# Optimization experiments

Hardware: AMD Instinct MI355X
Metric: run time of the kernel (lower is better)

Reference implementation:

```python
import jax, jax.numpy as jnp
from jax import lax
import numpy as np

THRESHOLD = 0.8
SECONDARY = 0.6
SECONDARY_WEIGHT = 0.5
BN_EPS = 1e-5


def _conv_relu_pool(x, W, b):
    # x: [B,C,H,W], W: [O,I,3,3]
    y = lax.conv_general_dilated(x, W, window_strides=(1, 1), padding='SAME',
                                 dimension_numbers=('NCHW', 'OIHW', 'NCHW'))
    y = y + b[None, :, None, None]
    y = jax.nn.relu(y)
    return lax.reduce_window(y, -jnp.inf, lax.max, (1, 1, 2, 2), (1, 1, 2, 2), 'VALID')


def setup_inputs() -> dict:
    key = jax.random.key(0)
    ks = jax.random.split(key, 12)
    B, H, W = 1024, 64, 64
    d0, d1, d2 = 4096, 1024, 256  # qnn_arch
    inp = {}
    inp['x'] = jax.random.normal(ks[0], (B, 1, H, W), dtype=jnp.float32)
    # conv params (kaiming-ish scaling)
    inp['cw1'] = jax.random.normal(ks[1], (8, 1, 3, 3), jnp.float32) * (1.0 / np.sqrt(1 * 9))
    inp['cb1'] = jax.random.normal(ks[2], (8,), jnp.float32) * 0.01
    inp['cw2'] = jax.random.normal(ks[3], (16, 8, 3, 3), jnp.float32) * (1.0 / np.sqrt(8 * 9))
    inp['cb2'] = jax.random.normal(ks[4], (16,), jnp.float32) * 0.01
    # linear layers of the 'graph QNN'
    inp['w1'] = jax.random.normal(ks[5], (d1, d0), jnp.float32) * (1.0 / np.sqrt(d0))
    inp['b1'] = jax.random.normal(ks[6], (d1,), jnp.float32) * 0.01
    inp['w2'] = jax.random.normal(ks[7], (d2, d1), jnp.float32) * (1.0 / np.sqrt(d1))
    inp['b2'] = jax.random.normal(ks[8], (d2,), jnp.float32) * 0.01
    # BatchNorm1d affine params
    inp['gamma'] = jnp.ones((d2,), jnp.float32)
    inp['beta'] = jnp.zeros((d2,), jnp.float32)
    return inp


def reference(x, cw1, cb1, cw2, cb2, w1, b1, w2, b2, gamma, beta):
    B = x.shape[0]
    # CNN feature extractor
    feat = _conv_relu_pool(x, cw1, cb1)
    feat = _conv_relu_pool(feat, cw2, cb2)
    flat = feat.reshape(B, -1)                      # [B, 4096]
    # graph-QNN layers with tanh
    h1 = jnp.tanh(flat @ w1.T + b1)                 # [B, 1024]
    last = jnp.tanh(h1 @ w2.T + b2)                 # [B, 256]
    # fidelity adjacency: vectorized normalize + Gram + squared cosine
    norms = jnp.linalg.norm(last, axis=1, keepdims=True)  # [B,1]
    nrm = last / (norms + 1e-12)
    fid = (nrm @ nrm.T) ** 2                        # [B, B]
    adj = jnp.where(fid >= THRESHOLD, 1.0,
                    jnp.where(fid >= SECONDARY, SECONDARY_WEIGHT, 0.0))
    adj = adj * (1.0 - jnp.eye(B, dtype=adj.dtype))  # no self-edges
    # BatchNorm1d (training mode: batch statistics, biased variance)
    mean = jnp.mean(last, axis=0)
    var = jnp.mean((last - mean) ** 2, axis=0)
    out = (last - mean) / jnp.sqrt(var + BN_EPS) * gamma + beta
    return out, adj
```

## Files before the change

### kernel.cpp

```cpp
#include <hip/hip_runtime.h>
#include <hip/hip_bf16.h>
#include <math.h>


typedef double f64x4 __attribute__((ext_vector_type(4)));

__global__ __launch_bounds__(256) void conv1_kernel(
    const float* __restrict__ x, const float* __restrict__ cw1,
    const float* __restrict__ cb1, float* __restrict__ feat1) {
  __shared__ float sX[66 * 66];
  __shared__ float sW1[72];
  __shared__ float sB1[8];

  const int b = blockIdx.x;
  const int t = threadIdx.x;

  for (int i = t; i < 66 * 66; i += 256) sX[i] = 0.0f;
  if (t < 72) sW1[t] = cw1[t];
  if (t < 8)  sB1[t] = cb1[t];
  __syncthreads();

  const float* xb = x + (size_t)b * 4096;
  for (int i = t; i < 4096; i += 256)
    sX[((i >> 6) + 1) * 66 + (i & 63) + 1] = xb[i];
  __syncthreads();

  for (int task = t; task < 2048; task += 256) {
    const int ch = task >> 8;
    const int rem = task & 255;
    const int py = rem >> 3;
    const int px0 = (rem & 7) * 4;

    double w9[9];
#pragma unroll
    for (int k = 0; k < 9; ++k) w9[k] = (double)sW1[ch * 9 + k];

    float reg[4][10];
#pragma unroll
    for (int r = 0; r < 4; ++r)
#pragma unroll
      for (int c = 0; c < 5; ++c) {
        const float2 v =
            *(const float2*)&sX[(2 * py + r) * 66 + 2 * px0 + 2 * c];
        reg[r][2 * c] = v.x;
        reg[r][2 * c + 1] = v.y;
      }

    float out4[4];
#pragma unroll
    for (int px = 0; px < 4; ++px) {
      double best = -1e300;
#pragma unroll
      for (int dy = 0; dy < 2; ++dy) {
#pragma unroll
        for (int dx = 0; dx < 2; ++dx) {
          double s = 0.0;
#pragma unroll
          for (int ky = 0; ky < 3; ++ky)
#pragma unroll
            for (int kx = 0; kx < 3; ++kx)
              s = fma((double)reg[dy + ky][2 * px + dx + kx], w9[ky * 3 + kx],
                      s);
          best = fmax(best, s);
        }
      }
      out4[px] = (float)fmax(best + (double)sB1[ch], 0.0);
    }
    *(float4*)&feat1[(size_t)b * 8192 + ch * 1024 + py * 32 + px0] =
        make_float4(out4[0], out4[1], out4[2], out4[3]);
  }
}

__global__ __launch_bounds__(256) void conv2_kernel(
    const float* __restrict__ feat1, const float* __restrict__ cw2,
    const float* __restrict__ cb2, float* __restrict__ flat) {
  __shared__ float sF[8 * 34 * 34];
  __shared__ float sW2[1152];
  __shared__ float sB2[16];

  const int b = blockIdx.x;
  const int t = threadIdx.x;

  for (int i = t; i < 8 * 34 * 34; i += 256) sF[i] = 0.0f;
  for (int i = t; i < 1152; i += 256) sW2[i] = cw2[i];
  if (t < 16) sB2[t] = cb2[t];
  __syncthreads();

  const float* fb = feat1 + (size_t)b * 8192;
  for (int i = t; i < 8192; i += 256) {
    const int ch = i >> 10, pos = i & 1023;
    sF[ch * 1156 + ((pos >> 5) + 1) * 34 + (pos & 31) + 1] = fb[i];
  }
  __syncthreads();

  const int py = t >> 4, px = t & 15;
  float* ob = flat + (size_t)b * 4096 + py * 16 + px;

#pragma unroll 1
  for (int oh = 0; oh < 2; ++oh) {
    double acc[8][4];
#pragma unroll
    for (int o = 0; o < 8; ++o)
#pragma unroll
      for (int q = 0; q < 4; ++q) acc[o][q] = 0.0;

#pragma unroll
    for (int ic = 0; ic < 8; ++ic) {
      float r[4][4];
#pragma unroll
      for (int iy = 0; iy < 4; ++iy) {
        const float2 v0 =
            *(const float2*)&sF[ic * 1156 + (2 * py + iy) * 34 + 2 * px];
        const float2 v1 =
            *(const float2*)&sF[ic * 1156 + (2 * py + iy) * 34 + 2 * px + 2];
        r[iy][0] = v0.x; r[iy][1] = v0.y; r[iy][2] = v1.x; r[iy][3] = v1.y;
      }
#pragma unroll
      for (int o = 0; o < 8; ++o) {
        const float* w = &sW2[(oh * 8 + o) * 72 + ic * 9];
        double w9[9];
#pragma unroll
        for (int k = 0; k < 9; ++k) w9[k] = (double)w[k];
#pragma unroll
        for (int dy = 0; dy < 2; ++dy)
#pragma unroll
          for (int dx = 0; dx < 2; ++dx) {
            double s = acc[o][dy * 2 + dx];
#pragma unroll
            for (int ky = 0; ky < 3; ++ky)
#pragma unroll
              for (int kx = 0; kx < 3; ++kx)
                s = fma((double)r[dy + ky][dx + kx], w9[ky * 3 + kx], s);
            acc[o][dy * 2 + dx] = s;
          }
      }
    }
#pragma unroll
    for (int o = 0; o < 8; ++o) {
      const int oc = oh * 8 + o;
      const double best =
          fmax(fmax(acc[o][0], acc[o][1]), fmax(acc[o][2], acc[o][3]));
      ob[oc * 256] = (float)fmax(best + (double)sB2[oc], 0.0);
    }
  }
}

__global__ __launch_bounds__(256) void conv_fused(
    const float* __restrict__ x,
    const float* __restrict__ cw1, const float* __restrict__ cb1,
    const float* __restrict__ cw2, const float* __restrict__ cb2,
    float* __restrict__ flat) {
  __shared__ float sX[66 * 66];
  __shared__ float sF[8 * 34 * 34];
  __shared__ float sW1[72];
  __shared__ float sW2[1152];
  __shared__ float sB1[8];
  __shared__ float sB2[16];

  const int b = blockIdx.x;
  const int t = threadIdx.x;

  for (int i = t; i < 66 * 66; i += 256) sX[i] = 0.0f;
  for (int i = t; i < 8 * 34 * 34; i += 256) sF[i] = 0.0f;
  if (t < 72) sW1[t] = cw1[t];
  for (int i = t; i < 1152; i += 256) sW2[i] = cw2[i];
  if (t < 8)  sB1[t] = cb1[t];
  if (t < 16) sB2[t] = cb2[t];
  __syncthreads();

  const float* xb = x + (size_t)b * 4096;
  for (int i = t; i < 4096; i += 256)
    sX[((i >> 6) + 1) * 66 + (i & 63) + 1] = xb[i];
  __syncthreads();

  for (int p = t; p < 8192; p += 256) {
    const int ch = p >> 10, pos = p & 1023;
    const int py1 = pos >> 5, px1 = pos & 31;
    double best = -1e300;
#pragma unroll
    for (int dy = 0; dy < 2; ++dy)
#pragma unroll
      for (int dx = 0; dx < 2; ++dx) {
        const int y = 2 * py1 + dy, xx = 2 * px1 + dx;
        double s = 0.0;
#pragma unroll
        for (int ky = 0; ky < 3; ++ky)
#pragma unroll
          for (int kx = 0; kx < 3; ++kx)
            s = fma((double)sX[(y + ky) * 66 + xx + kx],
                    (double)sW1[ch * 9 + ky * 3 + kx], s);
        best = fmax(best, s);
      }
    sF[ch * 1156 + (py1 + 1) * 34 + px1 + 1] =
        (float)fmax(best + (double)sB1[ch], 0.0);
  }
  __syncthreads();

  const int py = t >> 4, px = t & 15;
  for (int oh = 0; oh < 2; ++oh) {
    double acc[8][4];
#pragma unroll
    for (int o = 0; o < 8; ++o)
#pragma unroll
      for (int q = 0; q < 4; ++q) acc[o][q] = 0.0;
#pragma unroll
    for (int ic = 0; ic < 8; ++ic) {
      double r[4][4];
#pragma unroll
      for (int iy = 0; iy < 4; ++iy)
#pragma unroll
        for (int ix = 0; ix < 4; ++ix)
          r[iy][ix] = (double)sF[ic * 1156 + (2 * py + iy) * 34 + 2 * px + ix];
#pragma unroll
      for (int o = 0; o < 8; ++o) {
        const float* w = &sW2[(oh * 8 + o) * 72 + ic * 9];
        double w9[9];
#pragma unroll
        for (int k = 0; k < 9; ++k) w9[k] = (double)w[k];
#pragma unroll
        for (int dy = 0; dy < 2; ++dy)
#pragma unroll
          for (int dx = 0; dx < 2; ++dx) {
            double s = acc[o][dy * 2 + dx];
#pragma unroll
            for (int ky = 0; ky < 3; ++ky)
#pragma unroll
              for (int kx = 0; kx < 3; ++kx)
                s = fma(r[dy + ky][dx + kx], w9[ky * 3 + kx], s);
            acc[o][dy * 2 + dx] = s;
          }
      }
    }
    float* ob = flat + (size_t)b * 4096 + py * 16 + px;
#pragma unroll
    for (int o = 0; o < 8; ++o) {
      const int oc = oh * 8 + o;
      double best =
          fmax(fmax(acc[o][0], acc[o][1]), fmax(acc[o][2], acc[o][3]));
      ob[oc * 256] = (float)fmax(best + (double)sB2[oc], 0.0);
    }
  }
}

__global__ __launch_bounds__(256, 2) void gemm_mfma_128(
    const float* __restrict__ A, const float* __restrict__ B,
    double* __restrict__ P, int M, int N, int K, int Kc) {
  __shared__ double As[16][131];
  __shared__ double Bs[16][131];

  const int t = threadIdx.x;
  const int n0 = blockIdx.x * 128;
  const int m0 = blockIdx.y * 128;
  const int s  = blockIdx.z;
  const int kb = s * Kc;
  const int rS = t >> 2;
  const int cS = (t & 3) * 4;
  const int w  = t >> 6;
  const int lane = t & 63;
  const int lq = lane >> 4;
  const int ln = lane & 15;
  const int mW = (w >> 1) * 64;
  const int nW = (w & 1) * 64;

  f64x4 acc[4][4];
#pragma unroll
  for (int g = 0; g < 4; ++g)
#pragma unroll
    for (int h = 0; h < 4; ++h) acc[g][h] = {0.0, 0.0, 0.0, 0.0};

  const float* Alo = &A[(size_t)(m0 + rS) * K + cS];
  const float* Ahi = &A[(size_t)(m0 + 64 + rS) * K + cS];
  const float* Blo = &B[(size_t)(n0 + rS) * K + cS];
  const float* Bhi = &B[(size_t)(n0 + 64 + rS) * K + cS];

  float4 a0 = *(const float4*)&Alo[kb];
  float4 a1 = *(const float4*)&Ahi[kb];
  float4 b0 = *(const float4*)&Blo[kb];
  float4 b1 = *(const float4*)&Bhi[kb];

  for (int k0 = kb; k0 < kb + Kc; k0 += 16) {
    __syncthreads();
    As[cS + 0][rS] = (double)a0.x; As[cS + 1][rS] = (double)a0.y;
    As[cS + 2][rS] = (double)a0.z; As[cS + 3][rS] = (double)a0.w;
    As[cS + 0][64 + rS] = (double)a1.x; As[cS + 1][64 + rS] = (double)a1.y;
    As[cS + 2][64 + rS] = (double)a1.z; As[cS + 3][64 + rS] = (double)a1.w;
    Bs[cS + 0][rS] = (double)b0.x; Bs[cS + 1][rS] = (double)b0.y;
    Bs[cS + 2][rS] = (double)b0.z; Bs[cS + 3][rS] = (double)b0.w;
    Bs[cS + 0][64 + rS] = (double)b1.x; Bs[cS + 1][64 + rS] = (double)b1.y;
    Bs[cS + 2][64 + rS] = (double)b1.z; Bs[cS + 3][64 + rS] = (double)b1.w;
    if (k0 + 16 < kb + Kc) {
      a0 = *(const float4*)&Alo[k0 + 16];
      a1 = *(const float4*)&Ahi[k0 + 16];
      b0 = *(const float4*)&Blo[k0 + 16];
      b1 = *(const float4*)&Bhi[k0 + 16];
    }
    __syncthreads();
#pragma unroll
    for (int kq = 0; kq < 4; ++kq) {
      const int kr = 4 * kq + lq;
      double aF[4], bF[4];
#pragma unroll
      for (int g = 0; g < 4; ++g) aF[g] = As[kr][mW + 16 * g + ln];
#pragma unroll
      for (int h = 0; h < 4; ++h) bF[h] = Bs[kr][nW + 16 * h + ln];
#pragma unroll
      for (int g = 0; g < 4; ++g)
#pragma unroll
        for (int h = 0; h < 4; ++h)
          acc[g][h] = __builtin_amdgcn_mfma_f64_16x16x4f64(aF[g], bF[h],
                                                           acc[g][h], 0, 0, 0);
    }
  }

  double* Pp = P + (size_t)s * M * N;
#pragma unroll
  for (int g = 0; g < 4; ++g) {
#pragma unroll
    for (int h = 0; h < 4; ++h) {
#pragma unroll
      for (int v = 0; v < 4; ++v) {
        const int row = m0 + mW + 16 * g + 4 * lq + v;
        const int col = n0 + nW + 16 * h + ln;
        Pp[(size_t)row * N + col] = acc[g][h][v];
      }
    }
  }
}

__global__ __launch_bounds__(256) void reduce_tanh(
    const double* __restrict__ P, int S, const float* __restrict__ bias,
    float* __restrict__ C, int N, int total) {
  const int idx = blockIdx.x * 256 + threadIdx.x;
  if (idx >= total) return;
  double sum = 0.0;
  for (int s = 0; s < S; ++s) sum += P[(size_t)s * total + idx];
  const float zg = (float)sum;
  const float z = zg + bias[idx & (N - 1)];
  C[idx] = (float)tanh((double)z);
}

__global__ __launch_bounds__(256) void reduce_tanh_norm(
    const double* __restrict__ P, int S, const float* __restrict__ bias,
    float* __restrict__ last, float* __restrict__ nrm) {
  const int b = blockIdx.x;
  const int t = threadIdx.x;
  const int idx = b * 256 + t;
  const int total = 1024 * 256;
  double sum = 0.0;
  for (int s = 0; s < S; ++s) sum += P[(size_t)s * total + idx];
  const float zg = (float)sum;
  const float z = zg + bias[t];
  const float v = (float)tanh((double)z);
  last[idx] = v;

  const float sq = v * v;
  double s = (double)sq;
#pragma unroll
  for (int o = 32; o > 0; o >>= 1) s += __shfl_down(s, o);
  __shared__ double red[4];
  if ((t & 63) == 0) red[t >> 6] = s;
  __syncthreads();
  const double totalSq = red[0] + red[1] + red[2] + red[3];
  const float s32 = (float)totalSq;
  const float den = sqrtf(s32) + 1e-12f;
  nrm[idx] = v / den;
}

__global__ __launch_bounds__(256) void gram_adj_direct(
    const float* __restrict__ Nrm, float* __restrict__ adj, int Msz, int K) {
  __shared__ double As[16][66];
  __shared__ double Bs[16][66];

  const int t = threadIdx.x;
  const int n0 = blockIdx.x * 64;
  const int m0 = blockIdx.y * 64;
  const int lm = t >> 2;
  const int lk4 = (t & 3) * 4;
  const int ty = t >> 4;
  const int tx = t & 15;

  double acc[4][4];
#pragma unroll
  for (int i = 0; i < 4; ++i)
#pragma unroll
    for (int j = 0; j < 4; ++j) acc[i][j] = 0.0;

  for (int k0 = 0; k0 < K; k0 += 16) {
    const float4 av = *(const float4*)&Nrm[(size_t)(m0 + lm) * K + k0 + lk4];
    const float4 bv = *(const float4*)&Nrm[(size_t)(n0 + lm) * K + k0 + lk4];
    __syncthreads();
    As[lk4 + 0][lm] = (double)av.x; As[lk4 + 1][lm] = (double)av.y;
    As[lk4 + 2][lm] = (double)av.z; As[lk4 + 3][lm] = (double)av.w;
    Bs[lk4 + 0][lm] = (double)bv.x; Bs[lk4 + 1][lm] = (double)bv.y;
    Bs[lk4 + 2][lm] = (double)bv.z; Bs[lk4 + 3][lm] = (double)bv.w;
    __syncthreads();
#pragma unroll
    for (int k = 0; k < 16; ++k) {
      const double2 a01 = *(const double2*)&As[k][2 * ty];
      const double2 a23 = *(const double2*)&As[k][32 + 2 * ty];
      const double2 b01 = *(const double2*)&Bs[k][2 * tx];
      const double2 b23 = *(const double2*)&Bs[k][32 + 2 * tx];
      const double ar[4] = {a01.x, a01.y, a23.x, a23.y};
      const double br[4] = {b01.x, b01.y, b23.x, b23.y};
#pragma unroll
      for (int i = 0; i < 4; ++i)
#pragma unroll
        for (int j = 0; j < 4; ++j)
          acc[i][j] = fma(ar[i], br[j], acc[i][j]);
    }
  }

  const int rows[4] = {m0 + 2 * ty, m0 + 2 * ty + 1,
                       m0 + 32 + 2 * ty, m0 + 32 + 2 * ty + 1};
  const int cols[4] = {n0 + 2 * tx, n0 + 2 * tx + 1,
                       n0 + 32 + 2 * tx, n0 + 32 + 2 * tx + 1};
#pragma unroll
  for (int i = 0; i < 4; ++i)
#pragma unroll
    for (int j = 0; j < 4; ++j) {
      const float g = (float)acc[i][j];
      const float fid = g * g;
      float v = (fid >= 0.8f) ? 1.0f : ((fid >= 0.6f) ? 0.5f : 0.0f);
      if (rows[i] == cols[j]) v = 0.0f;
      adj[(size_t)rows[i] * Msz + cols[j]] = v;
    }
}

__global__ __launch_bounds__(256) void bn_stats(
    const float* __restrict__ last, const float* __restrict__ gamma,
    const float* __restrict__ beta, float* __restrict__ out) {
  const int j = blockIdx.x;
  const int t = threadIdx.x;
  double v[4];
  double s = 0.0;
#pragma unroll
  for (int i = 0; i < 4; ++i) {
    v[i] = (double)last[(size_t)(i * 256 + t) * 256 + j];
    s += v[i];
  }
#pragma unroll
  for (int o = 32; o > 0; o >>= 1) s += __shfl_down(s, o);
  __shared__ double red[4];
  if ((t & 63) == 0) red[t >> 6] = s;
  __syncthreads();
  const double mean = (red[0] + red[1] + red[2] + red[3]) * (1.0 / 1024.0);
  double q = 0.0;
#pragma unroll
  for (int i = 0; i < 4; ++i) {
    const double d = v[i] - mean;
    q += d * d;
  }
#pragma unroll
  for (int o = 32; o > 0; o >>= 1) q += __shfl_down(q, o);
  __syncthreads();
  if ((t & 63) == 0) red[t >> 6] = q;
  __syncthreads();
  const double var = (red[0] + red[1] + red[2] + red[3]) * (1.0 / 1024.0);
  const double g = (double)gamma[j] / sqrt(var + 1e-5);
  const double be = (double)beta[j];
#pragma unroll
  for (int i = 0; i < 4; ++i)
    out[(size_t)(i * 256 + t) * 256 + j] = (float)((v[i] - mean) * g + be);
}

extern "C" void kernel_launch(void* const* d_in, const int* in_sizes, int n_in,
                              void* d_out, int out_size, void* d_ws,
                              size_t ws_size, hipStream_t stream) {
  const float* x     = (const float*)d_in[0];
  const float* cw1   = (const float*)d_in[1];
  const float* cb1   = (const float*)d_in[2];
  const float* cw2   = (const float*)d_in[3];
  const float* cb2   = (const float*)d_in[4];
  const float* w1    = (const float*)d_in[5];
  const float* b1    = (const float*)d_in[6];
  const float* w2    = (const float*)d_in[7];
  const float* b2    = (const float*)d_in[8];
  const float* gamma = (const float*)d_in[9];
  const float* beta  = (const float*)d_in[10];

  float* outp = (float*)d_out;
  float* adj  = outp + 1024 * 256;

  float* ws   = (float*)d_ws;
  float* flat = ws;
  float* h1   = ws + 4194304;
  float* last = ws + 5242880;
  float* nrm  = ws + 5505024;
  double* part = (double*)(ws + 5767168);
  float* feat1 = (float*)part;

  const size_t baseB = 5767168ull * 4ull;
  int S1;
  if (ws_size >= baseB + 8ull * 1024 * 1024 * 8) S1 = 8;
  else if (ws_size >= baseB + 4ull * 1024 * 1024 * 8) S1 = 4;
  else S1 = 2;
  const int S2 = (S1 >= 4) ? 16 : 4;
  const bool split_conv = (S1 >= 4);

  if (split_conv) {
    conv1_kernel<<<1024, 256, 0, stream>>>(x, cw1, cb1, feat1);
    conv2_kernel<<<1024, 256, 0, stream>>>(feat1, cw2, cb2, flat);
  } else {
    conv_fused<<<1024, 256, 0, stream>>>(x, cw1, cb1, cw2, cb2, flat);
  }

  gemm_mfma_128<<<dim3(8, 8, S1), 256, 0, stream>>>(
      flat, w1, part, 1024, 1024, 4096, 4096 / S1);
  reduce_tanh<<<4096, 256, 0, stream>>>(part, S1, b1, h1, 1024, 1024 * 1024);

  gemm_mfma_128<<<dim3(2, 8, S2), 256, 0, stream>>>(
      h1, w2, part, 1024, 256, 1024, 1024 / S2);
  reduce_tanh_norm<<<1024, 256, 0, stream>>>(part, S2, b2, last, nrm);

  gram_adj_direct<<<dim3(16, 16), 256, 0, stream>>>(nrm, adj, 1024, 256);

  bn_stats<<<256, 256, 0, stream>>>(last, gamma, beta, outp);
}
```

Baseline: 395.1 us.

## Replace FP64 first GEMM with Ozaki-style int8 split MFMA emulation

Adds a prep kernel that scales each row of flat and w1 by a power of two and splits the values into four int8 slices. A new int8 MFMA GEMM then accumulates the cross-slice products in int32 and recombines them in double, with bias and tanh fused into the epilogue. This replaces the FP64 MFMA split-K GEMM and its separate reduction pass, aiming to use the much higher int8 MFMA throughput. In exchange it runs 13 MFMAs per tile step, adds a quantization pass over both matrices, and gives slightly different rounding from a true FP64 product.

Result: no change. 394.0 us (-0.3%).

```diff
diff --git a/kernel.cpp b/kernel.cpp
--- a/kernel.cpp
+++ b/kernel.cpp
@@ -4,6 +4,16 @@
 
 
 typedef double f64x4 __attribute__((ext_vector_type(4)));
+typedef int v4i __attribute__((ext_vector_type(4)));
+
+#if defined(__has_builtin)
+#if __has_builtin(__builtin_amdgcn_mfma_i32_16x16x64_i8)
+#define HAVE_I8_MFMA 1
+#endif
+#endif
+#ifndef HAVE_I8_MFMA
+#define HAVE_I8_MFMA 0
+#endif
 
 __global__ __launch_bounds__(256) void conv1_kernel(
     const float* __restrict__ x, const float* __restrict__ cw1,
@@ -327,6 +337,166 @@
   }
 }
 
+__global__ __launch_bounds__(256) void ozaki_prep(
+    const float* __restrict__ A, const float* __restrict__ B,
+    signed char* __restrict__ planes, double* __restrict__ scales) {
+  const int r = blockIdx.x;
+  const int mat = r >> 10;
+  const int row = r & 1023;
+  const float* src = (mat ? B : A) + (size_t)row * 4096;
+  const int t = threadIdx.x;
+
+  float mx = 0.0f;
+  for (int k = t; k < 4096; k += 256) mx = fmaxf(mx, fabsf(src[k]));
+#pragma unroll
+  for (int o = 32; o > 0; o >>= 1) mx = fmaxf(mx, __shfl_down(mx, o));
+  __shared__ float red[4];
+  if ((t & 63) == 0) red[t >> 6] = mx;
+  __syncthreads();
+  mx = fmaxf(fmaxf(red[0], red[1]), fmaxf(red[2], red[3]));
+
+  const int e = (mx > 0.0f) ? (ilogbf(mx) + 1) : 0;
+  const double qs = ldexp(1.0, 30 - e);
+  if (t == 0) scales[r] = ldexp(1.0, e - 30);
+
+  signed char* p0 = planes + (size_t)(mat * 4) * 4194304 + (size_t)row * 4096;
+  for (int k = t; k < 4096; k += 256) {
+    const int q = (int)lrint((double)src[k] * qs);
+    const int q1 = (q + (1 << 23)) >> 24;  const int r1 = q - (q1 << 24);
+    const int q2 = (r1 + (1 << 16)) >> 17; const int r2 = r1 - (q2 << 17);
+    const int q3 = (r2 + (1 << 9)) >> 10;  const int r3 = r2 - (q3 << 10);
+    const int q4 = (r3 + (1 << 2)) >> 3;
+    p0[k] = (signed char)q1;
+    p0[4194304 + k] = (signed char)q2;
+    p0[2 * 4194304 + k] = (signed char)q3;
+    p0[3 * 4194304 + k] = (signed char)q4;
+  }
+}
+
+#if HAVE_I8_MFMA
+__global__ __launch_bounds__(256, 1) void gemm1_i8(
+    const signed char* __restrict__ planes, const double* __restrict__ scales,
+    const float* __restrict__ bias, float* __restrict__ h1) {
+  __shared__ signed char sA[4][64][80];
+  __shared__ signed char sB[4][64][80];
+
+  const int t = threadIdx.x;
+  const int n0 = blockIdx.x * 64;
+  const int m0 = blockIdx.y * 64;
+  const int w = t >> 6;
+  const int lane = t & 63;
+  const int lq = lane >> 4;
+  const int ln = lane & 15;
+  const int mW = (w >> 1) * 32;
+  const int nW = (w & 1) * 32;
+  const int rowS = t >> 2;
+  const int kS = (t & 3) * 16;
+
+  v4i acc[4][5];
+#pragma unroll
+  for (int p = 0; p < 4; ++p)
+#pragma unroll
+    for (int g = 0; g < 5; ++g) acc[p][g] = (v4i){0, 0, 0, 0};
+
+  const signed char* pA = planes;
+  const signed char* pB = planes + 4ull * 4194304;
+
+  v4i pa[4], pb[4];
+#pragma unroll
+  for (int sl = 0; sl < 4; ++sl) {
+    pa[sl] = *(const v4i*)(pA + (size_t)sl * 4194304 +
+                           (size_t)(m0 + rowS) * 4096 + kS);
+    pb[sl] = *(const v4i*)(pB + (size_t)sl * 4194304 +
+                           (size_t)(n0 + rowS) * 4096 + kS);
+  }
+
+  for (int k0 = 0; k0 < 4096; k0 += 64) {
+    __syncthreads();
+#pragma unroll
+    for (int sl = 0; sl < 4; ++sl) {
+      *(v4i*)&sA[sl][rowS][kS] = pa[sl];
+      *(v4i*)&sB[sl][rowS][kS] = pb[sl];
+    }
+    if (k0 + 64 < 4096) {
+#pragma unroll
+      for (int sl = 0; sl < 4; ++sl) {
+        pa[sl] = *(const v4i*)(pA + (size_t)sl * 4194304 +
+                               (size_t)(m0 + rowS) * 4096 + k0 + 64 + kS);
+        pb[sl] = *(const v4i*)(pB + (size_t)sl * 4194304 +
+                               (size_t)(n0 + rowS) * 4096 + k0 + 64 + kS);
+      }
+    }
+    __syncthreads();
+
+    v4i aF[2][4], bF[2][4];
+#pragma unroll
+    for (int g = 0; g < 2; ++g)
+#pragma unroll
+      for (int sl = 0; sl < 4; ++sl)
+        aF[g][sl] = *(const v4i*)&sA[sl][mW + 16 * g + ln][lq * 16];
+#pragma unroll
+    for (int h = 0; h < 2; ++h)
+#pragma unroll
+      for (int sl = 0; sl < 4; ++sl)
+        bF[h][sl] = *(const v4i*)&sB[sl][nW + 16 * h + ln][lq * 16];
+
+#pragma unroll
+    for (int g = 0; g < 2; ++g) {
+#pragma unroll
+      for (int h = 0; h < 2; ++h) {
+        const int p = g * 2 + h;
+        acc[p][0] = __builtin_amdgcn_mfma_i32_16x16x64_i8(
+            aF[g][0], bF[h][0], acc[p][0], 0, 0, 0);
+        acc[p][1] = __builtin_amdgcn_mfma_i32_16x16x64_i8(
+            aF[g][0], bF[h][1], acc[p][1], 0, 0, 0);
+        acc[p][1] = __builtin_amdgcn_mfma_i32_16x16x64_i8(
+            aF[g][1], bF[h][0], acc[p][1], 0, 0, 0);
+        acc[p][2] = __builtin_amdgcn_mfma_i32_16x16x64_i8(
+            aF[g][0], bF[h][2], acc[p][2], 0, 0, 0);
+        acc[p][2] = __builtin_amdgcn_mfma_i32_16x16x64_i8(
+            aF[g][1], bF[h][1], acc[p][2], 0, 0, 0);
+        acc[p][2] = __builtin_amdgcn_mfma_i32_16x16x64_i8(
+            aF[g][2], bF[h][0], acc[p][2], 0, 0, 0);
+        acc[p][3] = __builtin_amdgcn_mfma_i32_16x16x64_i8(
+            aF[g][0], bF[h][3], acc[p][3], 0, 0, 0);
+        acc[p][3] = __builtin_amdgcn_mfma_i32_16x16x64_i8(
+            aF[g][1], bF[h][2], acc[p][3], 0, 0, 0);
+        acc[p][3] = __builtin_amdgcn_mfma_i32_16x16x64_i8(
+            aF[g][2], bF[h][1], acc[p][3], 0, 0, 0);
+        acc[p][3] = __builtin_amdgcn_mfma_i32_16x16x64_i8(
+            aF[g][3], bF[h][0], acc[p][3], 0, 0, 0);
+        acc[p][4] = __builtin_amdgcn_mfma_i32_16x16x64_i8(
+            aF[g][1], bF[h][3], acc[p][4], 0, 0, 0);
+        acc[p][4] = __builtin_amdgcn_mfma_i32_16x16x64_i8(
+            aF[g][2], bF[h][2], acc[p][4], 0, 0, 0);
+        acc[p][4] = __builtin_amdgcn_mfma_i32_16x16x64_i8(
+            aF[g][3], bF[h][1], acc[p][4], 0, 0, 0);
+      }
+    }
+  }
+
+#pragma unroll
+  for (int g = 0; g < 2; ++g) {
+#pragma unroll
+    for (int h = 0; h < 2; ++h) {
+      const int p = g * 2 + h;
+#pragma unroll
+      for (int v = 0; v < 4; ++v) {
+        const int row = m0 + mW + 16 * g + 4 * lq + v;
+        const int col = n0 + nW + 16 * h + ln;
+        const double sum = scales[row] * scales[1024 + col] *
+            ((double)acc[p][0][v] * 0x1p48 + (double)acc[p][1][v] * 0x1p41 +
+             (double)acc[p][2][v] * 0x1p34 + (double)acc[p][3][v] * 0x1p27 +
+             (double)acc[p][4][v] * 0x1p20);
+        const float zg = (float)sum;
+        const float z = zg + bias[col];
+        h1[(size_t)row * 1024 + col] = (float)tanh((double)z);
+      }
+    }
+  }
+}
+#endif
+
 __global__ __launch_bounds__(256) void reduce_tanh(
     const double* __restrict__ P, int S, const float* __restrict__ bias,
     float* __restrict__ C, int N, int total) {
@@ -481,33 +651,46 @@
   float* outp = (float*)d_out;
   float* adj  = outp + 1024 * 256;
 
-  float* ws   = (float*)d_ws;
-  float* flat = ws;
-  float* h1   = ws + 4194304;
-  float* last = ws + 5242880;
-  float* nrm  = ws + 5505024;
-  double* part = (double*)(ws + 5767168);
-  float* feat1 = (float*)part;
-
-  const size_t baseB = 5767168ull * 4ull;
-  int S1;
-  if (ws_size >= baseB + 8ull * 1024 * 1024 * 8) S1 = 8;
-  else if (ws_size >= baseB + 4ull * 1024 * 1024 * 8) S1 = 4;
-  else S1 = 2;
-  const int S2 = (S1 >= 4) ? 16 : 4;
-  const bool split_conv = (S1 >= 4);
-
-  if (split_conv) {
+  float* ws    = (float*)d_ws;
+  float* flat  = ws;
+  float* h1    = ws + 4194304;
+  float* last  = ws + 5242880;
+  float* nrm   = ws + 5505024;
+  double* scal = (double*)(ws + 5767168);
+  float* region = ws + 5771264;
+  float* feat1 = region;
+  signed char* planes = (signed char*)region;
+  double* part = (double*)region;
+
+  const size_t needB = 5771264ull * 4ull + 33554432ull;
+  const bool full = (ws_size >= needB);
+
+  if (full) {
     conv1_kernel<<<1024, 256, 0, stream>>>(x, cw1, cb1, feat1);
     conv2_kernel<<<1024, 256, 0, stream>>>(feat1, cw2, cb2, flat);
   } else {
     conv_fused<<<1024, 256, 0, stream>>>(x, cw1, cb1, cw2, cb2, flat);
   }
 
-  gemm_mfma_128<<<dim3(8, 8, S1), 256, 0, stream>>>(
-      flat, w1, part, 1024, 1024, 4096, 4096 / S1);
-  reduce_tanh<<<4096, 256, 0, stream>>>(part, S1, b1, h1, 1024, 1024 * 1024);
-
+#if HAVE_I8_MFMA
+  const bool use_i8 = full;
+#else
+  const bool use_i8 = false;
+#endif
+
+  if (use_i8) {
+#if HAVE_I8_MFMA
+    ozaki_prep<<<2048, 256, 0, stream>>>(flat, w1, planes, scal);
+    gemm1_i8<<<dim3(16, 16), 256, 0, stream>>>(planes, scal, b1, h1);
+#endif
+  } else {
+    const int S1 = full ? 8 : 2;
+    gemm_mfma_128<<<dim3(8, 8, S1), 256, 0, stream>>>(
+        flat, w1, part, 1024, 1024, 4096, 4096 / S1);
+    reduce_tanh<<<4096, 256, 0, stream>>>(part, S1, b1, h1, 1024, 1024 * 1024);
+  }
+
+  const int S2 = full ? 16 : 4;
   gemm_mfma_128<<<dim3(2, 8, S2), 256, 0, stream>>>(
       h1, w2, part, 1024, 256, 1024, 1024 / S2);
   reduce_tanh_norm<<<1024, 256, 0, stream>>>(part, S2, b2, last, nrm);
```
